# Optimization experiments

Measured on AMD Instinct MI355X. Metric: run time of the kernel, lower is better.

Reference implementation:

```python
import jax, jax.numpy as jnp
import numpy as np
import math

B, S, D, H, L, FF = 16, 512, 1024, 16, 4, 4096
DK = D // H
EPS = 1e-5
NEG = -1e32


def make_pe(max_len, d_model):
    pos = np.arange(max_len, dtype=np.float32)[:, None]
    div = np.exp(np.arange(0, d_model, 2, dtype=np.float32) * (-math.log(10000.0) / d_model))
    pe = np.zeros((max_len, d_model), dtype=np.float32)
    pe[:, 0::2] = np.sin(pos * div)
    pe[:, 1::2] = np.cos(pos * div)
    return jnp.asarray(pe[None])  # [1, max_len, d_model]


def setup_inputs() -> dict:
    key = jax.random.key(0)
    ks = jax.random.split(key, 32)
    sd = 0.02
    inp = {
        'q_embed_data': jax.random.normal(ks[0], (B, S, D), jnp.float32),
        'qa_embed_data': jax.random.normal(ks[1], (B, S, D), jnp.float32),
        'forget_rate': jax.random.uniform(ks[2], (B, 1, S, 1), jnp.float32),
        'pe': make_pe(S, D),
        'Wk': jax.random.normal(ks[3], (L, D, D), jnp.float32) * sd,
        'bk': jnp.zeros((L, D), jnp.float32),
        'Wv': jax.random.normal(ks[4], (L, D, D), jnp.float32) * sd,
        'bv': jnp.zeros((L, D), jnp.float32),
        'Wo': jax.random.normal(ks[5], (L, D, D), jnp.float32) * sd,
        'bo': jnp.zeros((L, D), jnp.float32),
        'W1': jax.random.normal(ks[6], (L, D, FF), jnp.float32) * sd,
        'b1': jnp.zeros((L, FF), jnp.float32),
        'W2': jax.random.normal(ks[7], (L, FF, D), jnp.float32) * sd,
        'b2': jnp.zeros((L, D), jnp.float32),
        'ln1_g': jnp.ones((L, D), jnp.float32),
        'ln1_b': jnp.zeros((L, D), jnp.float32),
        'ln2_g': jnp.ones((L, D), jnp.float32),
        'ln2_b': jnp.zeros((L, D), jnp.float32),
    }
    return inp


def layernorm(x, g, b):
    m = jnp.mean(x, -1, keepdims=True)
    v = jnp.mean((x - m) ** 2, -1, keepdims=True)
    return (x - m) * jax.lax.rsqrt(v + EPS) * g + b


def forward(q_embed_data, qa_embed_data, forget_rate, pe,
            Wk, bk, Wv, bv, Wo, bo, W1, b1, W2, b2,
            ln1_g, ln1_b, ln2_g, ln2_b):
    x = q_embed_data + pe[:, :S]
    y = qa_embed_data + pe[:, :S]
    # mask==0 path: allowed positions are strictly below diagonal (j < i)
    allowed = jnp.tril(jnp.ones((S, S), bool), k=-1)
    scale = 1.0 / math.sqrt(DK)
    for l in range(L):
        # kq_same: q also uses k_linear
        k = (x @ Wk[l] + bk[l]).reshape(B, S, H, DK).transpose(0, 2, 1, 3)
        q = k
        v = (y @ Wv[l] + bv[l]).reshape(B, S, H, DK).transpose(0, 2, 1, 3)
        scores = jnp.einsum('bhid,bhjd->bhij', q, k) * scale
        scores = scores * forget_rate  # [B,1,S,1] broadcasts over heads/cols
        scores = jnp.where(allowed, scores, NEG)
        attn = jax.nn.softmax(scores, axis=-1)
        attn = attn.at[:, :, 0, :].set(0.0)  # zero_pad of first query row
        out = jnp.einsum('bhij,bhjd->bhid', attn, v)
        out = out.transpose(0, 2, 1, 3).reshape(B, S, D) @ Wo[l] + bo[l]
        x = layernorm(x + out, ln1_g[l], ln1_b[l])
        ff = jax.nn.relu(x @ W1[l] + b1[l]) @ W2[l] + b2[l]
        x = layernorm(x + ff, ln2_g[l], ln2_b[l])
    return x


def reference(q_embed_data, qa_embed_data, forget_rate, pe,
              Wk, bk, Wv, bv, Wo, bo, W1, b1, W2, b2,
              ln1_g, ln1_b, ln2_g, ln2_b):
    return forward(q_embed_data, qa_embed_data, forget_rate, pe,
                   Wk, bk, Wv, bv, Wo, bo, W1, b1, W2, b2,
                   ln1_g, ln1_b, ln2_g, ln2_b)
```

## Files before the change

kernel.cpp:

```cpp
#include <hip/hip_runtime.h>
#include <hip/hip_bf16.h>
#include <cstdint>
#include <cstddef>

#define Bq 16
#define Sq 512
#define Dq 1024
#define Hq 16
#define Lq 4
#define FFq 4096
#define Mq (Bq * Sq)

typedef unsigned short ushort_t;
typedef __attribute__((ext_vector_type(8))) short short8;
typedef __attribute__((ext_vector_type(8))) unsigned short ushortx8;
typedef __attribute__((ext_vector_type(4))) unsigned short ushortx4;
typedef __attribute__((ext_vector_type(4))) float floatx4;

__device__ __forceinline__ float bf2f(ushort_t u) {
  union { unsigned int i; float f; } x;
  x.i = ((unsigned int)u) << 16;
  return x.f;
}
__device__ __forceinline__ ushort_t f2bf(float f) {
  unsigned int u = __float_as_uint(f);
  u += 0x7fffu + ((u >> 16) & 1u);
  return (ushort_t)(u >> 16);
}

#define GLL16(gp, lp) __builtin_amdgcn_global_load_lds( \
    (__attribute__((address_space(1))) void*)(gp),      \
    (__attribute__((address_space(3))) void*)(lp), 16, 0, 0)

__global__ void probe_kernel(const ushort_t* __restrict__ pe,
                             const ushort_t* __restrict__ g1,
                             int* __restrict__ flags)
{
  if (threadIdx.x == 0 && blockIdx.x == 0) {
    flags[0] = (pe[1] == (ushort_t)0x3F80u) ? 1 : 0;
    flags[1] = (g1[0] == (ushort_t)0x3F80u) ? 1 : 0;
  }
}

struct CvtArgs {
  const void* src[10];
  ushort_t*   dst[10];
  int         n[10];
  int         fi[10];
  int         cum[11];
};
__global__ __launch_bounds__(256) void convert_all_kernel(
    CvtArgs a, const int* __restrict__ flags)
{
  const int bidx = blockIdx.x;
  int s = 0;
  while (s < 9 && bidx >= a.cum[s + 1]) ++s;
  const int i = (bidx - a.cum[s]) * 256 + threadIdx.x;
  if (i >= a.n[s]) return;
  if (flags[a.fi[s]]) a.dst[s][i] = ((const ushort_t*)a.src[s])[i];
  else                a.dst[s][i] = f2bf(((const float*)a.src[s])[i]);
}

__global__ __launch_bounds__(256) void gemm_bt_kernel(
    const ushort_t* __restrict__ A, const ushort_t* __restrict__ BT,
    const ushort_t* __restrict__ bias, ushort_t* __restrict__ C,
    int N, int K, int relu)
{
  __shared__ __align__(16) ushort_t As[4][4096];
  __shared__ __align__(16) ushort_t Bs[4][4096];

  const int t = threadIdx.x;
  const int lane = t & 63;
  const int w = t >> 6;
  const int la = lane & 15;
  const int lb = lane >> 4;

  int bx = blockIdx.x, by = blockIdx.y;
  {
    const int gx = gridDim.x, gy = gridDim.y;
    if ((gy & 7) == 0) {
      const int orig = by * gx + bx;
      const int xcd = orig & 7;
      const int local = orig >> 3;
      const int rows = gy >> 3;
      by = xcd * rows + local % rows;
      bx = local / rows;
    }
  }
  const long m0 = (long)by * 128;
  const long n0 = (long)bx * 128;
  const int nk = K >> 5;

  const int f0 = (w << 7) + lane;
  const int f1 = f0 + 64;
  const int rA0 = f0 >> 2, rA1 = f1 >> 2;
  const int kA0 = ((f0 & 3) ^ ((rA0 >> 1) & 3)) << 3;
  const int kA1 = ((f1 & 3) ^ ((rA1 >> 1) & 3)) << 3;
  const ushort_t* gA0 = A + (m0 + rA0) * K + kA0;
  const ushort_t* gA1 = A + (m0 + rA1) * K + kA1;
  const ushort_t* gB0 = BT + (n0 + rA0) * K + kA0;
  const ushort_t* gB1 = BT + (n0 + rA1) * K + kA1;
  const int lo0 = (w * 2 + 0) * 512;
  const int lo1 = (w * 2 + 1) * 512;

  const floatx4 z4 = {0.f, 0.f, 0.f, 0.f};
  floatx4 acc[4][4];
#pragma unroll
  for (int i = 0; i < 4; ++i)
#pragma unroll
    for (int j = 0; j < 4; ++j) acc[i][j] = z4;

#define STAGE(buf, kt) do {                      \
    const long ko_ = (long)(kt) << 5;            \
    GLL16(gA0 + ko_, &As[(buf)][lo0]);           \
    GLL16(gA1 + ko_, &As[(buf)][lo1]);           \
    GLL16(gB0 + ko_, &Bs[(buf)][lo0]);           \
    GLL16(gB1 + ko_, &Bs[(buf)][lo1]);           \
  } while (0)

  STAGE(0, 0);
  STAGE(1, 1);
  STAGE(2, 2);

  const int wm = (w >> 1) * 64;
  const int wn = (w & 1) * 64;

  for (int kt = 0; kt < nk; ++kt) {
    const int rem = nk - 1 - kt;
    if (rem >= 2)      asm volatile("s_waitcnt vmcnt(8)" ::: "memory");
    else if (rem == 1) asm volatile("s_waitcnt vmcnt(4)" ::: "memory");
    else               asm volatile("s_waitcnt vmcnt(0)" ::: "memory");
    __builtin_amdgcn_s_barrier();

    const int cur = kt & 3;
    short8 af[4], bfr[4];
#pragma unroll
    for (int mf = 0; mf < 4; ++mf) {
      const int r = wm + mf * 16 + la;
      af[mf] = *(const short8*)&As[cur][r * 32 + ((lb ^ ((r >> 1) & 3)) << 3)];
    }
#pragma unroll
    for (int nf = 0; nf < 4; ++nf) {
      const int r = wn + nf * 16 + la;
      bfr[nf] = *(const short8*)&Bs[cur][r * 32 + ((lb ^ ((r >> 1) & 3)) << 3)];
    }
#pragma unroll
    for (int mf = 0; mf < 4; ++mf)
#pragma unroll
      for (int nf = 0; nf < 4; ++nf)
        acc[mf][nf] = __builtin_amdgcn_mfma_f32_16x16x32_bf16(af[mf], bfr[nf], acc[mf][nf], 0, 0, 0);

    asm volatile("s_waitcnt lgkmcnt(0)" ::: "memory");
    __builtin_amdgcn_s_barrier();
    if (kt + 3 < nk) STAGE((kt + 3) & 3, kt + 3);
  }
#undef STAGE

#pragma unroll
  for (int nf = 0; nf < 4; ++nf) {
    const long col = n0 + wn + nf * 16 + la;
    const float bsv = bf2f(bias[col]);
#pragma unroll
    for (int mf = 0; mf < 4; ++mf) {
      const long row = m0 + wm + mf * 16 + lb * 4;
      ushort_t* cp = C + row * N + col;
      const floatx4 v = acc[mf][nf];
#pragma unroll
      for (int r = 0; r < 4; ++r) {
        float x = v[r] + bsv;
        if (relu) x = fmaxf(x, 0.0f);
        cp[(long)r * N] = f2bf(x);
      }
    }
  }
}

__global__ __launch_bounds__(256) void attn_kernel(
    const ushort_t* __restrict__ kq, const ushort_t* __restrict__ vt,
    const ushort_t* __restrict__ fr, ushort_t* __restrict__ ao)
{
  __shared__ __align__(16) ushort_t P[4][64 * 72];
  const int t = threadIdx.x;
  const int lane = t & 63;
  const int w4 = t >> 6;
  const int wq = blockIdx.y * 4 + w4;
  const int b = blockIdx.x >> 4;
  const int h = blockIdx.x & 15;
  const int la = lane & 15;
  const int lb = lane >> 4;
  const int i0 = wq * 64;
  const long kbase = ((long)b * Sq) * Dq + h * 64;
  const long vbase = ((long)(b * Hq + h)) * (64L * Sq);

  short8 qf[4][2];
#pragma unroll
  for (int mf = 0; mf < 4; ++mf)
#pragma unroll
    for (int tt = 0; tt < 2; ++tt)
      qf[mf][tt] = *(const short8*)&kq[kbase + (long)(i0 + mf * 16 + la) * Dq + tt * 32 + lb * 8];

  float frs[4][4];
#pragma unroll
  for (int mf = 0; mf < 4; ++mf)
#pragma unroll
    for (int r = 0; r < 4; ++r)
      frs[mf][r] = 0.125f * bf2f(fr[b * Sq + i0 + mf * 16 + lb * 4 + r]);

  const floatx4 z4 = {0.f, 0.f, 0.f, 0.f};
  floatx4 o[4][4];
  float mrun[4][4], lrun[4][4];
#pragma unroll
  for (int mf = 0; mf < 4; ++mf)
#pragma unroll
    for (int x = 0; x < 4; ++x) {
      o[mf][x] = z4;
      mrun[mf][x] = -1e30f;
      lrun[mf][x] = 0.0f;
    }

  for (int jt = 0; jt <= wq; ++jt) {
    const int j0 = jt * 64;
    floatx4 s[4][4];
#pragma unroll
    for (int mf = 0; mf < 4; ++mf)
#pragma unroll
      for (int jf = 0; jf < 4; ++jf) s[mf][jf] = z4;

#pragma unroll
    for (int tt = 0; tt < 2; ++tt) {
      short8 kf[4];
#pragma unroll
      for (int jf = 0; jf < 4; ++jf)
        kf[jf] = *(const short8*)&kq[kbase + (long)(j0 + jf * 16 + la) * Dq + tt * 32 + lb * 8];
#pragma unroll
      for (int mf = 0; mf < 4; ++mf)
#pragma unroll
        for (int jf = 0; jf < 4; ++jf)
          s[mf][jf] = __builtin_amdgcn_mfma_f32_16x16x32_bf16(qf[mf][tt], kf[jf], s[mf][jf], 0, 0, 0);
    }

    const bool diag = (jt == wq);
#pragma unroll
    for (int mf = 0; mf < 4; ++mf)
#pragma unroll
      for (int jf = 0; jf < 4; ++jf)
#pragma unroll
        for (int r = 0; r < 4; ++r) {
          float x = s[mf][jf][r] * frs[mf][r];
          if (diag && (j0 + jf * 16 + la) >= (i0 + mf * 16 + lb * 4 + r)) x = -1e30f;
          s[mf][jf][r] = x;
        }

#pragma unroll
    for (int mf = 0; mf < 4; ++mf)
#pragma unroll
      for (int r = 0; r < 4; ++r) {
        float pm = fmaxf(fmaxf(s[mf][0][r], s[mf][1][r]), fmaxf(s[mf][2][r], s[mf][3][r]));
        pm = fmaxf(pm, __shfl_xor(pm, 1));
        pm = fmaxf(pm, __shfl_xor(pm, 2));
        pm = fmaxf(pm, __shfl_xor(pm, 4));
        pm = fmaxf(pm, __shfl_xor(pm, 8));
        const float mo = mrun[mf][r];
        const float mn = fmaxf(mo, pm);
        const float sc = __expf(mo - mn);
        mrun[mf][r] = mn;
        float rs = 0.0f;
#pragma unroll
        for (int jf = 0; jf < 4; ++jf) {
          const float p = __expf(s[mf][jf][r] - mn);
          s[mf][jf][r] = p;
          rs += p;
        }
        rs += __shfl_xor(rs, 1);
        rs += __shfl_xor(rs, 2);
        rs += __shfl_xor(rs, 4);
        rs += __shfl_xor(rs, 8);
        lrun[mf][r] = lrun[mf][r] * sc + rs;
#pragma unroll
        for (int df = 0; df < 4; ++df) o[mf][df][r] *= sc;
      }

#pragma unroll
    for (int mf = 0; mf < 4; ++mf)
#pragma unroll
      for (int jf = 0; jf < 4; ++jf)
#pragma unroll
        for (int r = 0; r < 4; ++r)
          P[w4][(mf * 16 + lb * 4 + r) * 72 + jf * 16 + la] = f2bf(s[mf][jf][r]);

#pragma unroll
    for (int tt = 0; tt < 2; ++tt) {
      short8 pf[4], vf[4];
#pragma unroll
      for (int mf = 0; mf < 4; ++mf)
        pf[mf] = *(const short8*)&P[w4][(mf * 16 + la) * 72 + tt * 32 + lb * 8];
#pragma unroll
      for (int df = 0; df < 4; ++df)
        vf[df] = *(const short8*)&vt[vbase + (long)(df * 16 + la) * Sq + j0 + tt * 32 + lb * 8];
#pragma unroll
      for (int mf = 0; mf < 4; ++mf)
#pragma unroll
        for (int df = 0; df < 4; ++df)
          o[mf][df] = __builtin_amdgcn_mfma_f32_16x16x32_bf16(pf[mf], vf[df], o[mf][df], 0, 0, 0);
    }
  }

#pragma unroll
  for (int mf = 0; mf < 4; ++mf)
#pragma unroll
    for (int df = 0; df < 4; ++df)
#pragma unroll
      for (int r = 0; r < 4; ++r) {
        const int ii = i0 + mf * 16 + lb * 4 + r;
        const float vv = (ii == 0) ? 0.0f : o[mf][df][r] / lrun[mf][r];
        ao[((long)b * Sq + ii) * Dq + h * 64 + df * 16 + la] = f2bf(vv);
      }
}

__global__ __launch_bounds__(256) void ln_kernel(
    float* __restrict__ xf, const ushort_t* __restrict__ add,
    const ushort_t* __restrict__ g, const ushort_t* __restrict__ bb,
    ushort_t* __restrict__ outb, float* __restrict__ outf,
    const int* __restrict__ flags, int final_)
{
  __shared__ float red[2][4];
  const long row = blockIdx.x;
  const int t = threadIdx.x;
  const int c = t * 4;
  float* xr = xf + row * Dq;
  const ushort_t* ar = add + row * Dq;

  floatx4 xv = *(floatx4*)&xr[c];
  ushortx4 av = *(const ushortx4*)&ar[c];
  float v[4];
  float s1 = 0.f, s2 = 0.f;
#pragma unroll
  for (int e = 0; e < 4; ++e) {
    v[e] = xv[e] + bf2f(av[e]);
    s1 += v[e];
    s2 += v[e] * v[e];
  }
#pragma unroll
  for (int m = 1; m < 64; m <<= 1) {
    s1 += __shfl_xor(s1, m);
    s2 += __shfl_xor(s2, m);
  }
  const int lane = t & 63, w = t >> 6;
  if (lane == 0) { red[0][w] = s1; red[1][w] = s2; }
  __syncthreads();
  s1 = red[0][0] + red[0][1] + red[0][2] + red[0][3];
  s2 = red[1][0] + red[1][1] + red[1][2] + red[1][3];
  const float mean = s1 * (1.0f / Dq);
  const float var = fmaxf(s2 * (1.0f / Dq) - mean * mean, 0.0f);
  const float rstd = rsqrtf(var + 1e-5f);
  ushortx4 gv = *(const ushortx4*)&g[c];
  ushortx4 bv = *(const ushortx4*)&bb[c];
  ushortx4 ob;
  floatx4 xo;
#pragma unroll
  for (int e = 0; e < 4; ++e) {
    const float y = (v[e] - mean) * rstd * bf2f(gv[e]) + bf2f(bv[e]);
    xo[e] = y;
    ob[e] = f2bf(y);
  }
  *(floatx4*)&xr[c] = xo;
  if (final_ && !flags[0]) {
    *(floatx4*)&outf[row * Dq + c] = xo;
  } else {
    *(ushortx4*)&outb[row * Dq + c] = ob;
  }
}

__global__ __launch_bounds__(256) void addpe_kernel(
    const void* __restrict__ qe, const void* __restrict__ qa,
    const void* __restrict__ pe, float* __restrict__ xf,
    ushort_t* __restrict__ xb, ushort_t* __restrict__ yb,
    const int* __restrict__ flags)
{
  const long i = ((long)blockIdx.x * 256 + threadIdx.x) * 8;
  const long sd = i & ((long)Sq * Dq - 1);
  const bool isb = flags[0] != 0;
  float q[8], a[8], p[8];
  if (isb) {
    ushortx8 q8 = *(const ushortx8*)((const ushort_t*)qe + i);
    ushortx8 a8 = *(const ushortx8*)((const ushort_t*)qa + i);
    ushortx8 p8 = *(const ushortx8*)((const ushort_t*)pe + sd);
#pragma unroll
    for (int e = 0; e < 8; ++e) { q[e] = bf2f(q8[e]); a[e] = bf2f(a8[e]); p[e] = bf2f(p8[e]); }
  } else {
    const float* qp = (const float*)qe + i;
    const float* ap = (const float*)qa + i;
    const float* pp = (const float*)pe + sd;
    floatx4 q0 = *(const floatx4*)qp, q1 = *(const floatx4*)(qp + 4);
    floatx4 a0 = *(const floatx4*)ap, a1 = *(const floatx4*)(ap + 4);
    floatx4 p0 = *(const floatx4*)pp, p1 = *(const floatx4*)(pp + 4);
#pragma unroll
    for (int e = 0; e < 4; ++e) {
      q[e] = q0[e]; q[e + 4] = q1[e];
      a[e] = a0[e]; a[e + 4] = a1[e];
      p[e] = p0[e]; p[e + 4] = p1[e];
    }
  }
  ushortx8 xo, yo;
  floatx4 f0, f1;
#pragma unroll
  for (int e = 0; e < 8; ++e) {
    const float xvv = (isb ? q[e] : bf2f(f2bf(q[e]))) + (isb ? p[e] : bf2f(f2bf(p[e])));
    const float yvv = (isb ? a[e] : bf2f(f2bf(a[e]))) + (isb ? p[e] : bf2f(f2bf(p[e])));
    if (e < 4) { f0[e] = xvv; } else { f1[e - 4] = xvv; }
    xo[e] = f2bf(xvv);
    yo[e] = f2bf(yvv);
  }
  *(floatx4*)&xf[i] = f0;
  *(floatx4*)&xf[i + 4] = f1;
  *(ushortx8*)&xb[i] = xo;
  *(ushortx8*)&yb[i] = yo;
}

__global__ __launch_bounds__(256) void transpose_kernel(
    const void* __restrict__ src, ushort_t* __restrict__ dst, int K, int N,
    const int* __restrict__ flags)
{
  __shared__ __align__(16) ushort_t tile[64][72];
  const bool isb = flags[1] != 0;
  const long base = (long)blockIdx.z * K * N;
  const int k0 = blockIdx.y * 64, n0 = blockIdx.x * 64;
  const int t = threadIdx.x;
  const int r = t >> 3;
  const int cc = (t & 7) << 3;
#pragma unroll
  for (int it = 0; it < 2; ++it) {
    const int rr = r + it * 32;
    const long gi = base + (long)(k0 + rr) * N + n0 + cc;
    if (isb) {
      *(short8*)&tile[rr][cc] = *(const short8*)((const ushort_t*)src + gi);
    } else {
      const float* sf = (const float*)src + gi;
      floatx4 v0 = *(const floatx4*)sf;
      floatx4 v1 = *(const floatx4*)(sf + 4);
#pragma unroll
      for (int e = 0; e < 4; ++e) {
        tile[rr][cc + e] = f2bf(v0[e]);
        tile[rr][cc + 4 + e] = f2bf(v1[e]);
      }
    }
  }
  __syncthreads();
#pragma unroll
  for (int it = 0; it < 2; ++it) {
    const int rr = r + it * 32;
    short8 v;
#pragma unroll
    for (int e = 0; e < 8; ++e) v[e] = (short)tile[cc + e][rr];
    *(short8*)&dst[base + (long)(n0 + rr) * K + k0 + cc] = v;
  }
}

__global__ __launch_bounds__(256) void vtrans_kernel(
    const ushort_t* __restrict__ vb, ushort_t* __restrict__ vt)
{
  __shared__ __align__(16) ushort_t tile[64][72];
  const int b = blockIdx.y >> 4, h = blockIdx.y & 15;
  const int j0 = blockIdx.x * 64;
  const int t = threadIdx.x;
  const int r = t >> 3;
  const int cc = (t & 7) << 3;
#pragma unroll
  for (int it = 0; it < 2; ++it) {
    const int rr = r + it * 32;
    *(short8*)&tile[rr][cc] = *(const short8*)&vb[((long)b * Sq + j0 + rr) * Dq + h * 64 + cc];
  }
  __syncthreads();
#pragma unroll
  for (int it = 0; it < 2; ++it) {
    const int rr = r + it * 32;
    short8 v;
#pragma unroll
    for (int e = 0; e < 8; ++e) v[e] = (short)tile[cc + e][rr];
    *(short8*)&vt[((long)(b * Hq + h) * 64 + rr) * Sq + j0 + cc] = v;
  }
}

extern "C" void kernel_launch(void* const* d_in, const int* in_sizes, int n_in,
                              void* d_out, int out_size, void* d_ws, size_t ws_size,
                              hipStream_t stream)
{
  if (n_in < 18) return;
  const void* qe  = d_in[0];
  const void* qa  = d_in[1];
  const void* fr  = d_in[2];
  const void* pe  = d_in[3];
  const void* Wk  = d_in[4];
  const void* bk  = d_in[5];
  const void* Wv  = d_in[6];
  const void* bv  = d_in[7];
  const void* Wo  = d_in[8];
  const void* bo  = d_in[9];
  const void* W1  = d_in[10];
  const void* b1  = d_in[11];
  const void* W2  = d_in[12];
  const void* b2  = d_in[13];
  const void* g1  = d_in[14];
  const void* be1 = d_in[15];
  const void* g2  = d_in[16];
  const void* be2 = d_in[17];

  char* ws = (char*)d_ws;
  const size_t SM = 243269632L;
  const size_t NEED = SM + 114752L;
  if (ws_size < NEED) return;

  float*    xf   = (float*)   (ws + 0L);
  ushort_t* xb   = (ushort_t*)(ws + 33554432L);
  ushort_t* yb   = (ushort_t*)(ws + 50331648L);
  ushort_t* tmpD = (ushort_t*)(ws + 67108864L);
  ushort_t* WkT  = (ushort_t*)(ws + 83886080L);
  ushort_t* WvT  = (ushort_t*)(ws + 92274688L);
  ushort_t* WoT  = (ushort_t*)(ws + 100663296L);
  ushort_t* W1T  = (ushort_t*)(ws + 109051904L);
  ushort_t* W2T  = (ushort_t*)(ws + 142606336L);
  ushort_t* kb   = (ushort_t*)(ws + 176160768L);
  ushort_t* vbf  = (ushort_t*)(ws + 192937984L);
  ushort_t* vtb  = (ushort_t*)(ws + 209715200L);
  ushort_t* ff1  = kb;

  int*      flags = (int*)(ws + SM);
  ushort_t* frc  = (ushort_t*)(ws + SM + 64);
  ushort_t* bkc  = (ushort_t*)(ws + SM + 16448);
  ushort_t* bvc  = (ushort_t*)(ws + SM + 24640);
  ushort_t* boc  = (ushort_t*)(ws + SM + 32832);
  ushort_t* b1c  = (ushort_t*)(ws + SM + 41024);
  ushort_t* b2c  = (ushort_t*)(ws + SM + 73792);
  ushort_t* g1c  = (ushort_t*)(ws + SM + 81984);
  ushort_t* be1c = (ushort_t*)(ws + SM + 90176);
  ushort_t* g2c  = (ushort_t*)(ws + SM + 98368);
  ushort_t* be2c = (ushort_t*)(ws + SM + 106560);

  probe_kernel<<<1, 64, 0, stream>>>((const ushort_t*)pe, (const ushort_t*)g1, flags);

  {
    CvtArgs a;
    const void* srcs[10] = {fr, bk, bv, bo, b1, b2, g1, be1, g2, be2};
    ushort_t*   dsts[10] = {frc, bkc, bvc, boc, b1c, b2c, g1c, be1c, g2c, be2c};
    const int   ns[10]   = {8192, 4096, 4096, 4096, 16384, 4096, 4096, 4096, 4096, 4096};
    int cum = 0;
    for (int s = 0; s < 10; ++s) {
      a.src[s] = srcs[s]; a.dst[s] = dsts[s]; a.n[s] = ns[s];
      a.fi[s] = (s == 0) ? 0 : 1;
      a.cum[s] = cum;
      cum += (ns[s] + 255) / 256;
    }
    a.cum[10] = cum;
    convert_all_kernel<<<cum, 256, 0, stream>>>(a, flags);
  }

  transpose_kernel<<<dim3(16, 16, 4), 256, 0, stream>>>(Wk, WkT, 1024, 1024, flags);
  transpose_kernel<<<dim3(16, 16, 4), 256, 0, stream>>>(Wv, WvT, 1024, 1024, flags);
  transpose_kernel<<<dim3(16, 16, 4), 256, 0, stream>>>(Wo, WoT, 1024, 1024, flags);
  transpose_kernel<<<dim3(64, 16, 4), 256, 0, stream>>>(W1, W1T, 1024, 4096, flags);
  transpose_kernel<<<dim3(16, 64, 4), 256, 0, stream>>>(W2, W2T, 4096, 1024, flags);

  addpe_kernel<<<4096, 256, 0, stream>>>(qe, qa, pe, xf, xb, yb, flags);

  for (int l = 0; l < 4; ++l) {
    gemm_bt_kernel<<<dim3(8, 64), 256, 0, stream>>>(xb, WkT + (long)l * 1048576, bkc + l * 1024, kb, 1024, 1024, 0);
    gemm_bt_kernel<<<dim3(8, 64), 256, 0, stream>>>(yb, WvT + (long)l * 1048576, bvc + l * 1024, vbf, 1024, 1024, 0);
    vtrans_kernel<<<dim3(8, 256), 256, 0, stream>>>(vbf, vtb);
    attn_kernel<<<dim3(256, 2), 256, 0, stream>>>(kb, vtb, frc, vbf);
    gemm_bt_kernel<<<dim3(8, 64), 256, 0, stream>>>(vbf, WoT + (long)l * 1048576, boc + l * 1024, tmpD, 1024, 1024, 0);
    ln_kernel<<<8192, 256, 0, stream>>>(xf, tmpD, g1c + l * 1024, be1c + l * 1024, xb, nullptr, flags, 0);
    gemm_bt_kernel<<<dim3(32, 64), 256, 0, stream>>>(xb, W1T + (long)l * 4194304, b1c + l * 4096, ff1, 4096, 1024, 1);
    gemm_bt_kernel<<<dim3(8, 64), 256, 0, stream>>>(ff1, W2T + (long)l * 4194304, b2c + l * 1024, tmpD, 1024, 4096, 0);
    if (l == 3) {
      ln_kernel<<<8192, 256, 0, stream>>>(xf, tmpD, g2c + l * 1024, be2c + l * 1024,
                                          (ushort_t*)d_out, (float*)d_out, flags, 1);
    } else {
      ln_kernel<<<8192, 256, 0, stream>>>(xf, tmpD, g2c + l * 1024, be2c + l * 1024,
                                          xb, nullptr, flags, 0);
    }
  }
}
```

Measured before the change: 1.879 ms.

## Shrink GEMM tile to 128x64, double-buffer LDS, batch K/V projections

Shrinks the GEMM block tile from 128x128 to 128x64. The four-deep asynchronous LDS pipeline with explicit vmcnt waits becomes a simple two-buffer scheme synchronised with __syncthreads. The kernel also takes a second set of operands chosen by blockIdx.z, so the K and V projections run in one launch. The aim is more, smaller blocks with less LDS each, for better occupancy and fewer launches. The cost is less operand reuse per LDS load and less latency hiding from the shallower prefetch.

```diff
diff --git a/kernel.cpp b/kernel.cpp
--- a/kernel.cpp
+++ b/kernel.cpp
@@ -62,12 +62,19 @@
 }
 
 __global__ __launch_bounds__(256) void gemm_bt_kernel(
-    const ushort_t* __restrict__ A, const ushort_t* __restrict__ BT,
-    const ushort_t* __restrict__ bias, ushort_t* __restrict__ C,
+    const ushort_t* __restrict__ A0, const ushort_t* __restrict__ BT0,
+    const ushort_t* __restrict__ bias0, ushort_t* __restrict__ C0,
+    const ushort_t* __restrict__ A1, const ushort_t* __restrict__ BT1,
+    const ushort_t* __restrict__ bias1, ushort_t* __restrict__ C1,
     int N, int K, int relu)
 {
-  __shared__ __align__(16) ushort_t As[4][4096];
-  __shared__ __align__(16) ushort_t Bs[4][4096];
+  __shared__ __align__(16) ushort_t As[2][128 * 32];
+  __shared__ __align__(16) ushort_t Bs[2][64 * 32];
+
+  const ushort_t* A    = blockIdx.z ? A1 : A0;
+  const ushort_t* BT   = blockIdx.z ? BT1 : BT0;
+  const ushort_t* bias = blockIdx.z ? bias1 : bias0;
+  ushort_t*       C    = blockIdx.z ? C1 : C0;
 
   const int t = threadIdx.x;
   const int lane = t & 63;
@@ -88,76 +95,69 @@
     }
   }
   const long m0 = (long)by * 128;
-  const long n0 = (long)bx * 128;
+  const long n0 = (long)bx * 64;
   const int nk = K >> 5;
 
-  const int f0 = (w << 7) + lane;
-  const int f1 = f0 + 64;
-  const int rA0 = f0 >> 2, rA1 = f1 >> 2;
-  const int kA0 = ((f0 & 3) ^ ((rA0 >> 1) & 3)) << 3;
-  const int kA1 = ((f1 & 3) ^ ((rA1 >> 1) & 3)) << 3;
-  const ushort_t* gA0 = A + (m0 + rA0) * K + kA0;
-  const ushort_t* gA1 = A + (m0 + rA1) * K + kA1;
-  const ushort_t* gB0 = BT + (n0 + rA0) * K + kA0;
-  const ushort_t* gB1 = BT + (n0 + rA1) * K + kA1;
-  const int lo0 = (w * 2 + 0) * 512;
-  const int lo1 = (w * 2 + 1) * 512;
-
-  const floatx4 z4 = {0.f, 0.f, 0.f, 0.f};
-  floatx4 acc[4][4];
-#pragma unroll
-  for (int i = 0; i < 4; ++i)
-#pragma unroll
-    for (int j = 0; j < 4; ++j) acc[i][j] = z4;
+  const int rA0 = t >> 2;
+  const int rA1 = 64 + (t >> 2);
+  const int cg  = t & 3;
+  const int cA0 = (cg ^ ((rA0 >> 1) & 3)) << 3;
+  const int cA1 = (cg ^ ((rA1 >> 1) & 3)) << 3;
+  const ushort_t* gA0 = A + (m0 + rA0) * K + cA0;
+  const ushort_t* gA1 = A + (m0 + rA1) * K + cA1;
+  const ushort_t* gB0 = BT + (n0 + rA0) * K + cA0;
+  const int loA0 = (w * 64) * 8;
+  const int loA1 = (256 + w * 64) * 8;
+  const int loB0 = (w * 64) * 8;
 
 #define STAGE(buf, kt) do {                      \
     const long ko_ = (long)(kt) << 5;            \
-    GLL16(gA0 + ko_, &As[(buf)][lo0]);           \
-    GLL16(gA1 + ko_, &As[(buf)][lo1]);           \
-    GLL16(gB0 + ko_, &Bs[(buf)][lo0]);           \
-    GLL16(gB1 + ko_, &Bs[(buf)][lo1]);           \
+    GLL16(gA0 + ko_, &As[(buf)][loA0]);          \
+    GLL16(gA1 + ko_, &As[(buf)][loA1]);          \
+    GLL16(gB0 + ko_, &Bs[(buf)][loB0]);          \
   } while (0)
 
+  const floatx4 z4 = {0.f, 0.f, 0.f, 0.f};
+  floatx4 acc[4][2];
+#pragma unroll
+  for (int i = 0; i < 4; ++i)
+#pragma unroll
+    for (int j = 0; j < 2; ++j) acc[i][j] = z4;
+
   STAGE(0, 0);
-  STAGE(1, 1);
-  STAGE(2, 2);
+  __syncthreads();
 
   const int wm = (w >> 1) * 64;
-  const int wn = (w & 1) * 64;
+  const int wn = (w & 1) * 32;
+  int cur = 0;
 
   for (int kt = 0; kt < nk; ++kt) {
-    const int rem = nk - 1 - kt;
-    if (rem >= 2)      asm volatile("s_waitcnt vmcnt(8)" ::: "memory");
-    else if (rem == 1) asm volatile("s_waitcnt vmcnt(4)" ::: "memory");
-    else               asm volatile("s_waitcnt vmcnt(0)" ::: "memory");
-    __builtin_amdgcn_s_barrier();
-
-    const int cur = kt & 3;
-    short8 af[4], bfr[4];
+    if (kt + 1 < nk) STAGE(cur ^ 1, kt + 1);
+
+    short8 af[4], bfr[2];
 #pragma unroll
     for (int mf = 0; mf < 4; ++mf) {
       const int r = wm + mf * 16 + la;
       af[mf] = *(const short8*)&As[cur][r * 32 + ((lb ^ ((r >> 1) & 3)) << 3)];
     }
 #pragma unroll
-    for (int nf = 0; nf < 4; ++nf) {
+    for (int nf = 0; nf < 2; ++nf) {
       const int r = wn + nf * 16 + la;
       bfr[nf] = *(const short8*)&Bs[cur][r * 32 + ((lb ^ ((r >> 1) & 3)) << 3)];
     }
 #pragma unroll
     for (int mf = 0; mf < 4; ++mf)
 #pragma unroll
-      for (int nf = 0; nf < 4; ++nf)
+      for (int nf = 0; nf < 2; ++nf)
         acc[mf][nf] = __builtin_amdgcn_mfma_f32_16x16x32_bf16(af[mf], bfr[nf], acc[mf][nf], 0, 0, 0);
 
-    asm volatile("s_waitcnt lgkmcnt(0)" ::: "memory");
-    __builtin_amdgcn_s_barrier();
-    if (kt + 3 < nk) STAGE((kt + 3) & 3, kt + 3);
+    __syncthreads();
+    cur ^= 1;
   }
 #undef STAGE
 
 #pragma unroll
-  for (int nf = 0; nf < 4; ++nf) {
+  for (int nf = 0; nf < 2; ++nf) {
     const long col = n0 + wn + nf * 16 + la;
     const float bsv = bf2f(bias[col]);
 #pragma unroll
@@ -563,14 +563,25 @@
   addpe_kernel<<<4096, 256, 0, stream>>>(qe, qa, pe, xf, xb, yb, flags);
 
   for (int l = 0; l < 4; ++l) {
-    gemm_bt_kernel<<<dim3(8, 64), 256, 0, stream>>>(xb, WkT + (long)l * 1048576, bkc + l * 1024, kb, 1024, 1024, 0);
-    gemm_bt_kernel<<<dim3(8, 64), 256, 0, stream>>>(yb, WvT + (long)l * 1048576, bvc + l * 1024, vbf, 1024, 1024, 0);
+    gemm_bt_kernel<<<dim3(16, 64, 2), 256, 0, stream>>>(
+        xb, WkT + (long)l * 1048576, bkc + l * 1024, kb,
+        yb, WvT + (long)l * 1048576, bvc + l * 1024, vbf,
+        1024, 1024, 0);
     vtrans_kernel<<<dim3(8, 256), 256, 0, stream>>>(vbf, vtb);
     attn_kernel<<<dim3(256, 2), 256, 0, stream>>>(kb, vtb, frc, vbf);
-    gemm_bt_kernel<<<dim3(8, 64), 256, 0, stream>>>(vbf, WoT + (long)l * 1048576, boc + l * 1024, tmpD, 1024, 1024, 0);
+    gemm_bt_kernel<<<dim3(16, 64, 1), 256, 0, stream>>>(
+        vbf, WoT + (long)l * 1048576, boc + l * 1024, tmpD,
+        vbf, WoT + (long)l * 1048576, boc + l * 1024, tmpD,
+        1024, 1024, 0);
     ln_kernel<<<8192, 256, 0, stream>>>(xf, tmpD, g1c + l * 1024, be1c + l * 1024, xb, nullptr, flags, 0);
-    gemm_bt_kernel<<<dim3(32, 64), 256, 0, stream>>>(xb, W1T + (long)l * 4194304, b1c + l * 4096, ff1, 4096, 1024, 1);
-    gemm_bt_kernel<<<dim3(8, 64), 256, 0, stream>>>(ff1, W2T + (long)l * 4194304, b2c + l * 1024, tmpD, 1024, 4096, 0);
+    gemm_bt_kernel<<<dim3(64, 64, 1), 256, 0, stream>>>(
+        xb, W1T + (long)l * 4194304, b1c + l * 4096, ff1,
+        xb, W1T + (long)l * 4194304, b1c + l * 4096, ff1,
+        4096, 1024, 1);
+    gemm_bt_kernel<<<dim3(16, 64, 1), 256, 0, stream>>>(
+        ff1, W2T + (long)l * 4194304, b2c + l * 1024, tmpD,
+        ff1, W2T + (long)l * 4194304, b2c + l * 1024, tmpD,
+        1024, 4096, 0);
     if (l == 3) {
       ln_kernel<<<8192, 256, 0, stream>>>(xf, tmpD, g2c + l * 1024, be2c + l * 1024,
                                           (ushort_t*)d_out, (float*)d_out, flags, 1);
```

Result: faster. 1.790 ms (-4.8%).
